# Kernel optimization log

Hardware: AMD Instinct MI355X
Metric: run time of the kernel (lower is better)

## Reference

```python
import jax, jax.numpy as jnp
import numpy as np

N = 50000      # nodes
E = 800000     # edges (avg degree 16)
IN = 128       # input feature dim
HID = 32       # per-head hidden dim
OUT = 64       # per-head output dim
H = 2          # heads per layer
NEG = 0.2      # leaky relu negative slope


def setup_inputs() -> dict:
    key = jax.random.key(0)
    ks = jax.random.split(key, 16)
    x = jax.random.normal(ks[0], (N, IN), dtype=jnp.float32)
    src = jax.random.randint(ks[1], (E,), 0, N)
    dst = jax.random.randint(ks[2], (E,), 0, N)

    def lin(k, fin, fout):
        return jax.random.normal(k, (fin, fout), dtype=jnp.float32) * (1.0 / np.sqrt(fin))

    def attn(k, h, d):
        return jax.random.normal(k, (h, d), dtype=jnp.float32) * 0.1

    # layer 0: IN -> H*HID, layer 1: H*HID -> H*HID, layer 2 (output): H*HID -> H*OUT
    W0, al0, ar0, b0 = lin(ks[3], IN, H * HID), attn(ks[4], H, HID), attn(ks[5], H, HID), jnp.zeros((H * HID,), jnp.float32)
    W1, al1, ar1, b1 = lin(ks[6], H * HID, H * HID), attn(ks[7], H, HID), attn(ks[8], H, HID), jnp.zeros((H * HID,), jnp.float32)
    W2, al2, ar2, b2 = lin(ks[9], H * HID, H * OUT), attn(ks[10], H, OUT), attn(ks[11], H, OUT), jnp.zeros((H * OUT,), jnp.float32)
    return {"x": x, "src": src, "dst": dst,
            "W0": W0, "al0": al0, "ar0": ar0, "b0": b0,
            "W1": W1, "al1": al1, "ar1": ar1, "b1": b1,
            "W2": W2, "al2": al2, "ar2": ar2, "b2": b2}


def gat_conv(x, src, dst, W, al, ar, b, heads, out_dim, apply_relu):
    # feat: [N, H, D]
    feat = (x @ W).reshape(-1, heads, out_dim)
    el = jnp.einsum('nhd,hd->nh', feat, al)   # [N, H]
    er = jnp.einsum('nhd,hd->nh', feat, ar)   # [N, H]
    # per-edge attention logits, leaky-relu
    e = jax.nn.leaky_relu(el[src] + er[dst], NEG)          # [E, H]
    # edge softmax over incoming edges of each dst node (numerically stable)
    m = jax.ops.segment_max(e, dst, num_segments=N)        # [N, H]
    m = jnp.where(jnp.isfinite(m), m, 0.0)                 # nodes w/o in-edges
    ex = jnp.exp(e - m[dst])                               # [E, H]
    s = jax.ops.segment_sum(ex, dst, num_segments=N)       # [N, H]
    alpha = ex / s[dst]                                    # [E, H]
    # weighted aggregate of source features into dst nodes
    rst = jax.ops.segment_sum(feat[src] * alpha[:, :, None], dst, num_segments=N)  # [N, H, D]
    rst = rst + b.reshape(1, heads, out_dim)
    if apply_relu:
        rst = jax.nn.relu(rst)
    return rst


def reference(x, src, dst, W0, al0, ar0, b0, W1, al1, ar1, b1, W2, al2, ar2, b2):
    h = gat_conv(x, src, dst, W0, al0, ar0, b0, H, HID, True).reshape(N, H * HID)   # flatten(1)
    h = gat_conv(h, src, dst, W1, al1, ar1, b1, H, HID, True).reshape(N, H * HID)   # flatten(1)
    logits = gat_conv(h, src, dst, W2, al2, ar2, b2, H, OUT, False).mean(axis=1)    # mean over heads -> [N, OUT]
    return logits
```

## Files before the change

kernel.cpp:

```cpp
#include <hip/hip_runtime.h>
#include <hip/hip_bf16.h>
#include <hip/hip_fp16.h>

#define NNODES 50000
#define NEG_SLOPE 0.2f
#define BKT_SHIFT 8
#define NBKT ((NNODES + 255) >> 8)
#define STRIDE 5120
#define PCHUNK 2048
#define PEPT 8

typedef _Float16 half8 __attribute__((ext_vector_type(8)));
typedef float v4f __attribute__((ext_vector_type(4)));

__device__ __forceinline__ int rfl(int v) { return __builtin_amdgcn_readfirstlane(v); }

__device__ __forceinline__ void pack_one(const float* W, _Float16* Wp, int K, int C, int tid) {
    int KC = K / 32;
    int l = tid & 63;
    int kc = (tid >> 6) % KC;
    int t = tid / (KC * 64);
    int cc = l & 15, q = l >> 4;
    half8 b;
#pragma unroll
    for (int j = 0; j < 8; j++)
        b[j] = (_Float16)W[(size_t)(kc * 32 + q * 8 + j) * C + t * 16 + cc];
    *(half8*)(Wp + (size_t)tid * 8) = b;
}

__global__ __launch_bounds__(256) void kernelAB(
    const float* __restrict__ x, const float* __restrict__ W0,
    const float* __restrict__ AL, const float* __restrict__ AR,
    _Float16* __restrict__ featA, float2* __restrict__ el2A, float2* __restrict__ er2A,
    const float* __restrict__ W2, _Float16* __restrict__ Wp2,
    const int* __restrict__ src, const int* __restrict__ dst,
    int* __restrict__ bcursor, int2* __restrict__ ebuf, int E, int N) {
    int blk = blockIdx.x;
    if (blk >= 786) {
        __shared__ int hist[NBKT];
        __shared__ int gbase[NBKT];
        int t = threadIdx.x;
        for (int i = t; i < NBKT; i += 256) hist[i] = 0;
        __syncthreads();
        int base = (blk - 786) * PCHUNK;
        int sreg[PEPT], dreg[PEPT], rreg[PEPT], breg[PEPT];
#pragma unroll
        for (int k = 0; k < PEPT; k++) {
            int i = base + k * 256 + t;
            if (i < E) {
                sreg[k] = src[i];
                dreg[k] = dst[i];
                breg[k] = dreg[k] >> BKT_SHIFT;
                rreg[k] = atomicAdd(&hist[breg[k]], 1);
            } else {
                breg[k] = -1;
            }
        }
        __syncthreads();
        for (int i = t; i < NBKT; i += 256)
            if (hist[i]) gbase[i] = i * STRIDE + atomicAdd(&bcursor[i * 16], hist[i]);
        __syncthreads();
#pragma unroll
        for (int k = 0; k < PEPT; k++) {
            if (breg[k] >= 0)
                ebuf[(size_t)(gbase[breg[k]] + rreg[k])] = make_int2(sreg[k], dreg[k]);
        }
        return;
    }
    if (blk >= 782) {
        int tid = (blk - 782) * 256 + threadIdx.x;
        if (tid < 8 * 2 * 64) pack_one(W2, Wp2, 64, 128, tid);
        return;
    }
    int wave = threadIdx.x >> 6, lane = threadIdx.x & 63;
    int mtile = blk * 4 + wave;
    if (mtile * 16 >= N) return;
    int m0 = mtile * 16;
    int c = lane & 15, q = lane >> 4;
    v4f acc[4];
#pragma unroll
    for (int t = 0; t < 4; t++) acc[t] = (v4f){0.f, 0.f, 0.f, 0.f};
    const size_t arow = (size_t)(m0 + c) * 128 + q * 8;
#pragma unroll
    for (int kc = 0; kc < 4; kc++) {
        const float* xr = x + arow + kc * 32;
        float4 f0 = *(const float4*)xr;
        float4 f1 = *(const float4*)(xr + 4);
        float fv[8] = {f0.x, f0.y, f0.z, f0.w, f1.x, f1.y, f1.z, f1.w};
        half8 ah, av;
#pragma unroll
        for (int j = 0; j < 8; j++) {
            ah[j] = (_Float16)fv[j];
            av[j] = (_Float16)(fv[j] - (float)ah[j]);
        }
#pragma unroll
        for (int tt = 0; tt < 4; tt++) {
            half8 b;
#pragma unroll
            for (int j = 0; j < 8; j++)
                b[j] = (_Float16)W0[(size_t)(kc * 32 + q * 8 + j) * 64 + tt * 16 + c];
            acc[tt] = __builtin_amdgcn_mfma_f32_16x16x32_f16(ah, b, acc[tt], 0, 0, 0);
            acc[tt] = __builtin_amdgcn_mfma_f32_16x16x32_f16(av, b, acc[tt], 0, 0, 0);
        }
    }
#pragma unroll
    for (int tt = 0; tt < 4; tt++)
#pragma unroll
        for (int r = 0; r < 4; r++) {
            int row = m0 + q * 4 + r;
            featA[(size_t)row * 64 + tt * 16 + c] = (_Float16)acc[tt][r];
        }
    float alv[4], arv[4];
#pragma unroll
    for (int tt = 0; tt < 4; tt++) { alv[tt] = AL[tt * 16 + c]; arv[tt] = AR[tt * 16 + c]; }
#pragma unroll
    for (int r = 0; r < 4; r++) {
        float l0 = 0.f, l1 = 0.f, r0 = 0.f, r1 = 0.f;
#pragma unroll
        for (int tt = 0; tt < 4; tt++) {
            float v = acc[tt][r];
            if (tt < 2) { l0 = fmaf(v, alv[tt], l0); r0 = fmaf(v, arv[tt], r0); }
            else        { l1 = fmaf(v, alv[tt], l1); r1 = fmaf(v, arv[tt], r1); }
        }
#pragma unroll
        for (int m = 1; m < 16; m <<= 1) {
            l0 += __shfl_xor(l0, m, 64);
            l1 += __shfl_xor(l1, m, 64);
            r0 += __shfl_xor(r0, m, 64);
            r1 += __shfl_xor(r1, m, 64);
        }
        if (c == 0) {
            int row = m0 + q * 4 + r;
            el2A[row] = make_float2(l0, l1);
            er2A[row] = make_float2(r0, r1);
        }
    }
}

__global__ __launch_bounds__(256) void local_sort(const int2* __restrict__ ebuf,
                                                  const int* __restrict__ bcursor,
                                                  int2* __restrict__ rowse,
                                                  int* __restrict__ csrc, int N) {
    __shared__ int lcnt[256], lrow[256], ws[4];
    int b = blockIdx.x;
    int d0 = b << BKT_SHIFT;
    int t = threadIdx.x;
    int base = b * STRIDE;
    int endE = base + bcursor[b * 16];
    lcnt[t] = 0;
    __syncthreads();
    for (int i = base + t; i < endE; i += 256)
        atomicAdd(&lcnt[ebuf[i].y - d0], 1);
    __syncthreads();
    int v = lcnt[t];
    int lane = t & 63;
    int x = v;
#pragma unroll
    for (int m = 1; m < 64; m <<= 1) {
        int y = __shfl_up(x, m, 64);
        if (lane >= m) x += y;
    }
    if (lane == 63) ws[t >> 6] = x;
    __syncthreads();
    int w = t >> 6, waveoff = 0;
#pragma unroll
    for (int k = 0; k < 4; k++) if (k < w) waveoff += ws[k];
    int excl = base + waveoff + x - v;
    lrow[t] = excl;
    int d = d0 + t;
    if (d < N) rowse[d] = make_int2(excl, excl + v);
    lcnt[t] = 0;
    __syncthreads();
    for (int i = base + t; i < endE; i += 256) {
        int2 e = ebuf[i];
        int ld = e.y - d0;
        int p = lrow[ld] + atomicAdd(&lcnt[ld], 1);
        csrc[p] = e.x;
    }
}

__global__ __launch_bounds__(256) void agg0_gemm1(
    const int2* __restrict__ rowse, const int* __restrict__ csrc,
    const float2* __restrict__ el2A, const float2* __restrict__ er2A,
    const _Float16* __restrict__ featA, const float* __restrict__ b0,
    const float* __restrict__ W1, const float* __restrict__ al1, const float* __restrict__ ar1,
    _Float16* __restrict__ featB, float2* __restrict__ el2B, float2* __restrict__ er2B,
    int N) {
    __shared__ int2 stA[4][64], stB[4][64];
    __shared__ float vbuf[4][64];
    __shared__ float4 w1v[16 * 64];
    int wave = threadIdx.x >> 6, lane = threadIdx.x & 63, h = lane >> 5;
    for (int i = threadIdx.x; i < 64 * 64; i += 256) {
        int k = i >> 6, cc = i & 63;
        ((float*)w1v)[((((k >> 2) << 6) + cc) << 2) | (k & 3)] = W1[i];
    }
    __syncthreads();
    float bl = b0[lane];
    float al1v = al1[lane], ar1v = ar1[lane];
    const int2* stH = h ? stB[wave] : stA[wave];
    for (int n0 = blockIdx.x * 4 + wave; n0 < N; n0 += gridDim.x * 4) {
        int n = rfl(n0);
        int2 se = rowse[n];
        int beg = rfl(se.x), end = rfl(se.y);
        float2 rr = er2A[n];
        float s = 0.f, acc = 0.f;
        for (int base = beg; base < end; base += 64) {
            int idx = base + lane;
            int sv = 0; float wxv = 0.f, wyv = 0.f;
            if (idx < end) {
                sv = csrc[idx];
                float2 l = el2A[sv];
                float t0 = l.x + rr.x; t0 = t0 > 0.f ? t0 : NEG_SLOPE * t0;
                float t1 = l.y + rr.y; t1 = t1 > 0.f ? t1 : NEG_SLOPE * t1;
                wxv = __expf(t0); wyv = __expf(t1);
            }
            stA[wave][lane] = make_int2(sv, __float_as_int(wxv));
            stB[wave][lane] = make_int2(sv, __float_as_int(wyv));
            int cnt = (min(64, end - base) + 7) & ~7;
            for (int j = 0; j < cnt; j += 8) {
                int4 e01 = *(const int4*)(stH + j);
                int4 e23 = *(const int4*)(stH + j + 2);
                int4 e45 = *(const int4*)(stH + j + 4);
                int4 e67 = *(const int4*)(stH + j + 6);
                float f0 = (float)featA[(size_t)e01.x * 64 + lane];
                float f1 = (float)featA[(size_t)e01.z * 64 + lane];
                float f2 = (float)featA[(size_t)e23.x * 64 + lane];
                float f3 = (float)featA[(size_t)e23.z * 64 + lane];
                float f4 = (float)featA[(size_t)e45.x * 64 + lane];
                float f5 = (float)featA[(size_t)e45.z * 64 + lane];
                float f6 = (float)featA[(size_t)e67.x * 64 + lane];
                float f7 = (float)featA[(size_t)e67.z * 64 + lane];
                float w0 = __int_as_float(e01.y), w1 = __int_as_float(e01.w);
                float w2 = __int_as_float(e23.y), w3 = __int_as_float(e23.w);
                float w4 = __int_as_float(e45.y), w5 = __int_as_float(e45.w);
                float w6 = __int_as_float(e67.y), w7 = __int_as_float(e67.w);
                s += ((w0 + w1) + (w2 + w3)) + ((w4 + w5) + (w6 + w7));
                acc = fmaf(w0, f0, acc);
                acc = fmaf(w1, f1, acc);
                acc = fmaf(w2, f2, acc);
                acc = fmaf(w3, f3, acc);
                acc = fmaf(w4, f4, acc);
                acc = fmaf(w5, f5, acc);
                acc = fmaf(w6, f6, acc);
                acc = fmaf(w7, f7, acc);
            }
        }
        float v = (s > 0.f) ? acc / s : 0.f;
        v = fmaxf(v + bl, 0.f);
        vbuf[wave][lane] = v;
        const float4* vv = (const float4*)vbuf[wave];
        float f = 0.f;
#pragma unroll
        for (int kk = 0; kk < 16; kk++) {
            float4 v4 = vv[kk];
            float4 w4 = w1v[(kk << 6) + lane];
            f = fmaf(v4.x, w4.x, f);
            f = fmaf(v4.y, w4.y, f);
            f = fmaf(v4.z, w4.z, f);
            f = fmaf(v4.w, w4.w, f);
        }
        featB[(size_t)n * 64 + lane] = (_Float16)f;
        float vl = f * al1v, vr = f * ar1v;
#pragma unroll
        for (int m = 1; m < 32; m <<= 1) {
            vl += __shfl_xor(vl, m, 64);
            vr += __shfl_xor(vr, m, 64);
        }
        if ((lane & 31) == 0) {
            ((float*)el2B)[n * 2 + h] = vl;
            ((float*)er2B)[n * 2 + h] = vr;
        }
    }
}

__global__ __launch_bounds__(256) void aggregate32(
    const int2* __restrict__ rowse, const int* __restrict__ csrc,
    const float2* __restrict__ el2, const float2* __restrict__ er2,
    const _Float16* __restrict__ feat16, const float* __restrict__ b,
    _Float16* __restrict__ ahi, _Float16* __restrict__ alo, int N) {
    __shared__ int2 stA[4][64], stB[4][64];
    int wave = threadIdx.x >> 6, lane = threadIdx.x & 63, h = lane >> 5;
    int n = rfl(blockIdx.x * 4 + wave);
    if (n >= N) return;
    float bl = b[lane];
    int2 se = rowse[n];
    int beg = rfl(se.x), end = rfl(se.y);
    float2 rr = er2[n];
    const int2* stH = h ? stB[wave] : stA[wave];
    float s = 0.f, acc = 0.f;
    for (int base = beg; base < end; base += 64) {
        int idx = base + lane;
        int sv = 0; float wxv = 0.f, wyv = 0.f;
        if (idx < end) {
            sv = csrc[idx];
            float2 l = el2[sv];
            float t0 = l.x + rr.x; t0 = t0 > 0.f ? t0 : NEG_SLOPE * t0;
            float t1 = l.y + rr.y; t1 = t1 > 0.f ? t1 : NEG_SLOPE * t1;
            wxv = __expf(t0); wyv = __expf(t1);
        }
        stA[wave][lane] = make_int2(sv, __float_as_int(wxv));
        stB[wave][lane] = make_int2(sv, __float_as_int(wyv));
        int cnt = (min(64, end - base) + 7) & ~7;
        for (int j = 0; j < cnt; j += 8) {
            int4 e01 = *(const int4*)(stH + j);
            int4 e23 = *(const int4*)(stH + j + 2);
            int4 e45 = *(const int4*)(stH + j + 4);
            int4 e67 = *(const int4*)(stH + j + 6);
            float f0 = (float)feat16[(size_t)e01.x * 64 + lane];
            float f1 = (float)feat16[(size_t)e01.z * 64 + lane];
            float f2 = (float)feat16[(size_t)e23.x * 64 + lane];
            float f3 = (float)feat16[(size_t)e23.z * 64 + lane];
            float f4 = (float)feat16[(size_t)e45.x * 64 + lane];
            float f5 = (float)feat16[(size_t)e45.z * 64 + lane];
            float f6 = (float)feat16[(size_t)e67.x * 64 + lane];
            float f7 = (float)feat16[(size_t)e67.z * 64 + lane];
            float w0 = __int_as_float(e01.y), w1 = __int_as_float(e01.w);
            float w2 = __int_as_float(e23.y), w3 = __int_as_float(e23.w);
            float w4 = __int_as_float(e45.y), w5 = __int_as_float(e45.w);
            float w6 = __int_as_float(e67.y), w7 = __int_as_float(e67.w);
            s += ((w0 + w1) + (w2 + w3)) + ((w4 + w5) + (w6 + w7));
            acc = fmaf(w0, f0, acc);
            acc = fmaf(w1, f1, acc);
            acc = fmaf(w2, f2, acc);
            acc = fmaf(w3, f3, acc);
            acc = fmaf(w4, f4, acc);
            acc = fmaf(w5, f5, acc);
            acc = fmaf(w6, f6, acc);
            acc = fmaf(w7, f7, acc);
        }
    }
    float v = (s > 0.f) ? acc / s : 0.f;
    v = fmaxf(v + bl, 0.f);
    _Float16 hv = (_Float16)v;
    ahi[(size_t)n * 64 + lane] = hv;
    alo[(size_t)n * 64 + lane] = (_Float16)(v - (float)hv);
}

__global__ __launch_bounds__(256) void gemm_mfma2(
    const _Float16* __restrict__ Ahi, const _Float16* __restrict__ Alo,
    const _Float16* __restrict__ Wp,
    const float* __restrict__ AL, const float* __restrict__ AR,
    __half2* __restrict__ feat2, float2* __restrict__ el2, float2* __restrict__ er2,
    int N) {
    constexpr int KC = 2, NT = 8;
    int wave = threadIdx.x >> 6, lane = threadIdx.x & 63;
    int mtile = blockIdx.x * 4 + wave;
    if (mtile * 16 >= N) return;
    int m0 = mtile * 16;
    int c = lane & 15, q = lane >> 4;
    v4f acc[NT];
#pragma unroll
    for (int t = 0; t < NT; t++) acc[t] = (v4f){0.f, 0.f, 0.f, 0.f};
    const size_t arow = (size_t)(m0 + c) * 64 + q * 8;
#pragma unroll
    for (int kc = 0; kc < KC; kc++) {
        half8 ah = *(const half8*)(Ahi + arow + kc * 32);
        half8 av = *(const half8*)(Alo + arow + kc * 32);
#pragma unroll
        for (int t = 0; t < NT; t++) {
            half8 b = *(const half8*)(Wp + ((size_t)(t * KC + kc) * 64 + lane) * 8);
            acc[t] = __builtin_amdgcn_mfma_f32_16x16x32_f16(ah, b, acc[t], 0, 0, 0);
            acc[t] = __builtin_amdgcn_mfma_f32_16x16x32_f16(av, b, acc[t], 0, 0, 0);
        }
    }
#pragma unroll
    for (int t = 0; t < NT / 2; t++)
#pragma unroll
        for (int r = 0; r < 4; r++) {
            int row = m0 + q * 4 + r;
            feat2[(size_t)row * 64 + t * 16 + c] =
                __floats2half2_rn(acc[t][r], acc[t + NT / 2][r]);
        }
    float alv[NT], arv[NT];
#pragma unroll
    for (int t = 0; t < NT; t++) { alv[t] = AL[t * 16 + c]; arv[t] = AR[t * 16 + c]; }
#pragma unroll
    for (int r = 0; r < 4; r++) {
        float l0 = 0.f, l1 = 0.f, r0 = 0.f, r1 = 0.f;
#pragma unroll
        for (int t = 0; t < NT; t++) {
            float v = acc[t][r];
            if (t < NT / 2) { l0 = fmaf(v, alv[t], l0); r0 = fmaf(v, arv[t], r0); }
            else            { l1 = fmaf(v, alv[t], l1); r1 = fmaf(v, arv[t], r1); }
        }
#pragma unroll
        for (int m = 1; m < 16; m <<= 1) {
            l0 += __shfl_xor(l0, m, 64);
            l1 += __shfl_xor(l1, m, 64);
            r0 += __shfl_xor(r0, m, 64);
            r1 += __shfl_xor(r1, m, 64);
        }
        if (c == 0) {
            int row = m0 + q * 4 + r;
            el2[row] = make_float2(l0, l1);
            er2[row] = make_float2(r0, r1);
        }
    }
}

__global__ __launch_bounds__(256) void aggregate64_mean(
    const int2* __restrict__ rowse, const int* __restrict__ csrc,
    const float2* __restrict__ el2, const float2* __restrict__ er2,
    const __half2* __restrict__ feat2, const float* __restrict__ b,
    float* __restrict__ out, int N) {
    __shared__ int4 st[4][64];
    int wave = threadIdx.x >> 6, lane = threadIdx.x & 63;
    int n = rfl(blockIdx.x * 4 + wave);
    if (n >= N) return;
    float b0 = b[lane], b1 = b[64 + lane];
    int2 se = rowse[n];
    int beg = rfl(se.x), end = rfl(se.y);
    float2 rr = er2[n];
    float s0 = 0.f, s1 = 0.f, a0 = 0.f, a1 = 0.f;
    for (int base = beg; base < end; base += 64) {
        int idx = base + lane;
        int sv = 0; float wxv = 0.f, wyv = 0.f;
        if (idx < end) {
            sv = csrc[idx];
            float2 l = el2[sv];
            float t0 = l.x + rr.x; t0 = t0 > 0.f ? t0 : NEG_SLOPE * t0;
            float t1 = l.y + rr.y; t1 = t1 > 0.f ? t1 : NEG_SLOPE * t1;
            wxv = __expf(t0); wyv = __expf(t1);
        }
        st[wave][lane] = make_int4(sv, __float_as_int(wxv), __float_as_int(wyv), 0);
        int cnt = (min(64, end - base) + 7) & ~7;
        for (int j = 0; j < cnt; j += 8) {
            float2 fv[8]; float wxs[8], wys[8];
#pragma unroll
            for (int u = 0; u < 8; u++) {
                int4 e = st[wave][j + u];
                wxs[u] = __int_as_float(e.y);
                wys[u] = __int_as_float(e.z);
                fv[u] = __half22float2(feat2[(size_t)e.x * 64 + lane]);
            }
#pragma unroll
            for (int u = 0; u < 8; u++) {
                s0 += wxs[u]; s1 += wys[u];
                a0 = fmaf(wxs[u], fv[u].x, a0);
                a1 = fmaf(wys[u], fv[u].y, a1);
            }
        }
    }
    float v0 = (s0 > 0.f) ? a0 / s0 : 0.f;
    float v1 = (s1 > 0.f) ? a1 / s1 : 0.f;
    out[(size_t)n * 64 + lane] = 0.5f * ((v0 + b0) + (v1 + b1));
}


extern "C" void kernel_launch(void* const* d_in, const int* in_sizes, int n_in,
                              void* d_out, int out_size, void* d_ws, size_t ws_size,
                              hipStream_t stream) {
    const float* x   = (const float*)d_in[0];
    const int*   src = (const int*)d_in[1];
    const int*   dst = (const int*)d_in[2];
    const float* W0  = (const float*)d_in[3];
    const float* al0 = (const float*)d_in[4];
    const float* ar0 = (const float*)d_in[5];
    const float* b0  = (const float*)d_in[6];
    const float* W1  = (const float*)d_in[7];
    const float* al1 = (const float*)d_in[8];
    const float* ar1 = (const float*)d_in[9];
    const float* b1  = (const float*)d_in[10];
    const float* W2  = (const float*)d_in[11];
    const float* al2 = (const float*)d_in[12];
    const float* ar2 = (const float*)d_in[13];
    const float* b2  = (const float*)d_in[14];
    float* out = (float*)d_out;

    const int N = NNODES;
    const int E = in_sizes[1];

    char* p = (char*)d_ws;
    auto alloc = [&](size_t bytes) {
        void* r = (void*)p;
        p += (bytes + 255) & ~(size_t)255;
        return r;
    };
    int*    bcursor = (int*)alloc((size_t)NBKT * 16 * 4);
    int2*   rowse   = (int2*)alloc((size_t)N * 8);
    int2*   ebuf    = (int2*)alloc(((size_t)NBKT * STRIDE + 4096) * 8);
    int*    csrc    = (int*)alloc(((size_t)NBKT * STRIDE + 4096) * 4);
    float2* el2A    = (float2*)alloc((size_t)N * 8);
    float2* er2A    = (float2*)alloc((size_t)N * 8);
    float2* el2B    = (float2*)alloc((size_t)N * 8);
    float2* er2B    = (float2*)alloc((size_t)N * 8);
    _Float16* ahi   = (_Float16*)alloc((size_t)N * 64 * 2);
    _Float16* alo   = (_Float16*)alloc((size_t)N * 64 * 2);
    void*   featA   = alloc((size_t)N * 64 * 4);
    _Float16* featB = (_Float16*)alloc((size_t)N * 64 * 2);
    _Float16* Wp2   = (_Float16*)alloc(8 * 2 * 64 * 8 * 2);

    hipMemsetAsync(bcursor, 0, (size_t)NBKT * 16 * 4, stream);
    int nch = (E + PCHUNK - 1) / PCHUNK;
    kernelAB<<<786 + nch, 256, 0, stream>>>(x, W0, al0, ar0, (_Float16*)featA, el2A, er2A,
                                            W2, Wp2, src, dst, bcursor, ebuf, E, N);
    local_sort<<<NBKT, 256, 0, stream>>>(ebuf, bcursor, rowse, csrc, N);

    int nb4 = (N + 3) / 4;
    agg0_gemm1<<<2048, 256, 0, stream>>>(rowse, csrc, el2A, er2A, (const _Float16*)featA,
                                         b0, W1, al1, ar1, featB, el2B, er2B, N);
    aggregate32<<<nb4, 256, 0, stream>>>(rowse, csrc, el2B, er2B, featB, b1, ahi, alo, N);
    int gb = (N / 16 + 3) / 4;
    gemm_mfma2<<<gb, 256, 0, stream>>>(ahi, alo, Wp2, al2, ar2, (__half2*)featA, el2A, er2A, N);
    aggregate64_mean<<<nb4, 256, 0, stream>>>(rowse, csrc, el2A, er2A, (const __half2*)featA,
                                              b2, out, N);
}
```

Before: 226.9 us.

## Process two destination nodes per wave in aggregation kernels, widen local sort

```diff
diff --git a/kernel.cpp b/kernel.cpp
--- a/kernel.cpp
+++ b/kernel.cpp
@@ -137,22 +137,22 @@
     }
 }
 
-__global__ __launch_bounds__(256) void local_sort(const int2* __restrict__ ebuf,
-                                                  const int* __restrict__ bcursor,
-                                                  int2* __restrict__ rowse,
-                                                  int* __restrict__ csrc, int N) {
+__global__ __launch_bounds__(1024) void local_sort(const int2* __restrict__ ebuf,
+                                                   const int* __restrict__ bcursor,
+                                                   int2* __restrict__ rowse,
+                                                   int* __restrict__ csrc, int N) {
     __shared__ int lcnt[256], lrow[256], ws[4];
     int b = blockIdx.x;
     int d0 = b << BKT_SHIFT;
     int t = threadIdx.x;
     int base = b * STRIDE;
     int endE = base + bcursor[b * 16];
-    lcnt[t] = 0;
+    if (t < 256) lcnt[t] = 0;
     __syncthreads();
-    for (int i = base + t; i < endE; i += 256)
+    for (int i = base + t; i < endE; i += 1024)
         atomicAdd(&lcnt[ebuf[i].y - d0], 1);
     __syncthreads();
-    int v = lcnt[t];
+    int v = (t < 256) ? lcnt[t] : 0;
     int lane = t & 63;
     int x = v;
 #pragma unroll
@@ -160,18 +160,20 @@
         int y = __shfl_up(x, m, 64);
         if (lane >= m) x += y;
     }
-    if (lane == 63) ws[t >> 6] = x;
+    if (t < 256 && lane == 63) ws[t >> 6] = x;
     __syncthreads();
-    int w = t >> 6, waveoff = 0;
-#pragma unroll
-    for (int k = 0; k < 4; k++) if (k < w) waveoff += ws[k];
-    int excl = base + waveoff + x - v;
-    lrow[t] = excl;
-    int d = d0 + t;
-    if (d < N) rowse[d] = make_int2(excl, excl + v);
-    lcnt[t] = 0;
+    if (t < 256) {
+        int w = t >> 6, waveoff = 0;
+#pragma unroll
+        for (int k = 0; k < 4; k++) if (k < w) waveoff += ws[k];
+        int excl = base + waveoff + x - v;
+        lrow[t] = excl;
+        int d = d0 + t;
+        if (d < N) rowse[d] = make_int2(excl, excl + v);
+        lcnt[t] = 0;
+    }
     __syncthreads();
-    for (int i = base + t; i < endE; i += 256) {
+    for (int i = base + t; i < endE; i += 1024) {
         int2 e = ebuf[i];
         int ld = e.y - d0;
         int p = lrow[ld] + atomicAdd(&lcnt[ld], 1);
@@ -278,34 +280,58 @@
     const float2* __restrict__ el2, const float2* __restrict__ er2,
     const _Float16* __restrict__ feat16, const float* __restrict__ b,
     _Float16* __restrict__ ahi, _Float16* __restrict__ alo, int N) {
-    __shared__ int2 stA[4][64], stB[4][64];
+    __shared__ int2 stA0[4][64], stB0[4][64], stA1[4][64], stB1[4][64];
     int wave = threadIdx.x >> 6, lane = threadIdx.x & 63, h = lane >> 5;
-    int n = rfl(blockIdx.x * 4 + wave);
-    if (n >= N) return;
+    int g = rfl(blockIdx.x * 4 + wave);
+    int n0 = 2 * g, n1 = n0 + 1;
+    if (n0 >= N) return;
+    bool has1 = (n1 < N);
     float bl = b[lane];
-    int2 se = rowse[n];
-    int beg = rfl(se.x), end = rfl(se.y);
-    float2 rr = er2[n];
-    const int2* stH = h ? stB[wave] : stA[wave];
-    float s = 0.f, acc = 0.f;
-    for (int base = beg; base < end; base += 64) {
-        int idx = base + lane;
-        int sv = 0; float wxv = 0.f, wyv = 0.f;
-        if (idx < end) {
-            sv = csrc[idx];
-            float2 l = el2[sv];
-            float t0 = l.x + rr.x; t0 = t0 > 0.f ? t0 : NEG_SLOPE * t0;
-            float t1 = l.y + rr.y; t1 = t1 > 0.f ? t1 : NEG_SLOPE * t1;
-            wxv = __expf(t0); wyv = __expf(t1);
-        }
-        stA[wave][lane] = make_int2(sv, __float_as_int(wxv));
-        stB[wave][lane] = make_int2(sv, __float_as_int(wyv));
-        int cnt = (min(64, end - base) + 7) & ~7;
+    int2 se0 = rowse[n0];
+    int2 se1 = has1 ? rowse[n1] : make_int2(0, 0);
+    int beg0 = rfl(se0.x), len0 = rfl(se0.y) - beg0;
+    int beg1 = rfl(se1.x), len1 = rfl(se1.y) - beg1;
+    float2 rr0 = er2[n0];
+    float2 rr1 = has1 ? er2[n1] : make_float2(0.f, 0.f);
+    const int2* stH0 = h ? stB0[wave] : stA0[wave];
+    const int2* stH1 = h ? stB1[wave] : stA1[wave];
+    float s0 = 0.f, acc0 = 0.f, s1 = 0.f, acc1 = 0.f;
+    int chunks = max(len0, len1);
+    for (int off = 0; off < chunks; off += 64) {
+        {
+            int sv = 0; float wxv = 0.f, wyv = 0.f;
+            if (off + lane < len0) {
+                sv = csrc[beg0 + off + lane];
+                float2 l = el2[sv];
+                float t0 = l.x + rr0.x; t0 = t0 > 0.f ? t0 : NEG_SLOPE * t0;
+                float t1 = l.y + rr0.y; t1 = t1 > 0.f ? t1 : NEG_SLOPE * t1;
+                wxv = __expf(t0); wyv = __expf(t1);
+            }
+            stA0[wave][lane] = make_int2(sv, __float_as_int(wxv));
+            stB0[wave][lane] = make_int2(sv, __float_as_int(wyv));
+        }
+        {
+            int sv = 0; float wxv = 0.f, wyv = 0.f;
+            if (off + lane < len1) {
+                sv = csrc[beg1 + off + lane];
+                float2 l = el2[sv];
+                float t0 = l.x + rr1.x; t0 = t0 > 0.f ? t0 : NEG_SLOPE * t0;
+                float t1 = l.y + rr1.y; t1 = t1 > 0.f ? t1 : NEG_SLOPE * t1;
+                wxv = __expf(t0); wyv = __expf(t1);
+            }
+            stA1[wave][lane] = make_int2(sv, __float_as_int(wxv));
+            stB1[wave][lane] = make_int2(sv, __float_as_int(wyv));
+        }
+        int cnt = (min(64, chunks - off) + 7) & ~7;
         for (int j = 0; j < cnt; j += 8) {
-            int4 e01 = *(const int4*)(stH + j);
-            int4 e23 = *(const int4*)(stH + j + 2);
-            int4 e45 = *(const int4*)(stH + j + 4);
-            int4 e67 = *(const int4*)(stH + j + 6);
+            int4 e01 = *(const int4*)(stH0 + j);
+            int4 e23 = *(const int4*)(stH0 + j + 2);
+            int4 e45 = *(const int4*)(stH0 + j + 4);
+            int4 e67 = *(const int4*)(stH0 + j + 6);
+            int4 g01 = *(const int4*)(stH1 + j);
+            int4 g23 = *(const int4*)(stH1 + j + 2);
+            int4 g45 = *(const int4*)(stH1 + j + 4);
+            int4 g67 = *(const int4*)(stH1 + j + 6);
             float f0 = (float)feat16[(size_t)e01.x * 64 + lane];
             float f1 = (float)feat16[(size_t)e01.z * 64 + lane];
             float f2 = (float)feat16[(size_t)e23.x * 64 + lane];
@@ -314,26 +340,54 @@
             float f5 = (float)feat16[(size_t)e45.z * 64 + lane];
             float f6 = (float)feat16[(size_t)e67.x * 64 + lane];
             float f7 = (float)feat16[(size_t)e67.z * 64 + lane];
+            float p0 = (float)feat16[(size_t)g01.x * 64 + lane];
+            float p1 = (float)feat16[(size_t)g01.z * 64 + lane];
+            float p2 = (float)feat16[(size_t)g23.x * 64 + lane];
+            float p3 = (float)feat16[(size_t)g23.z * 64 + lane];
+            float p4 = (float)feat16[(size_t)g45.x * 64 + lane];
+            float p5 = (float)feat16[(size_t)g45.z * 64 + lane];
+            float p6 = (float)feat16[(size_t)g67.x * 64 + lane];
+            float p7 = (float)feat16[(size_t)g67.z * 64 + lane];
             float w0 = __int_as_float(e01.y), w1 = __int_as_float(e01.w);
             float w2 = __int_as_float(e23.y), w3 = __int_as_float(e23.w);
             float w4 = __int_as_float(e45.y), w5 = __int_as_float(e45.w);
             float w6 = __int_as_float(e67.y), w7 = __int_as_float(e67.w);
-            s += ((w0 + w1) + (w2 + w3)) + ((w4 + w5) + (w6 + w7));
-            acc = fmaf(w0, f0, acc);
-            acc = fmaf(w1, f1, acc);
-            acc = fmaf(w2, f2, acc);
-            acc = fmaf(w3, f3, acc);
-            acc = fmaf(w4, f4, acc);
-            acc = fmaf(w5, f5, acc);
-            acc = fmaf(w6, f6, acc);
-            acc = fmaf(w7, f7, acc);
-        }
-    }
-    float v = (s > 0.f) ? acc / s : 0.f;
+            float x0 = __int_as_float(g01.y), x1 = __int_as_float(g01.w);
+            float x2 = __int_as_float(g23.y), x3 = __int_as_float(g23.w);
+            float x4 = __int_as_float(g45.y), x5 = __int_as_float(g45.w);
+            float x6 = __int_as_float(g67.y), x7 = __int_as_float(g67.w);
+            s0 += ((w0 + w1) + (w2 + w3)) + ((w4 + w5) + (w6 + w7));
+            acc0 = fmaf(w0, f0, acc0);
+            acc0 = fmaf(w1, f1, acc0);
+            acc0 = fmaf(w2, f2, acc0);
+            acc0 = fmaf(w3, f3, acc0);
+            acc0 = fmaf(w4, f4, acc0);
+            acc0 = fmaf(w5, f5, acc0);
+            acc0 = fmaf(w6, f6, acc0);
+            acc0 = fmaf(w7, f7, acc0);
+            s1 += ((x0 + x1) + (x2 + x3)) + ((x4 + x5) + (x6 + x7));
+            acc1 = fmaf(x0, p0, acc1);
+            acc1 = fmaf(x1, p1, acc1);
+            acc1 = fmaf(x2, p2, acc1);
+            acc1 = fmaf(x3, p3, acc1);
+            acc1 = fmaf(x4, p4, acc1);
+            acc1 = fmaf(x5, p5, acc1);
+            acc1 = fmaf(x6, p6, acc1);
+            acc1 = fmaf(x7, p7, acc1);
+        }
+    }
+    float v = (s0 > 0.f) ? acc0 / s0 : 0.f;
     v = fmaxf(v + bl, 0.f);
     _Float16 hv = (_Float16)v;
-    ahi[(size_t)n * 64 + lane] = hv;
-    alo[(size_t)n * 64 + lane] = (_Float16)(v - (float)hv);
+    ahi[(size_t)n0 * 64 + lane] = hv;
+    alo[(size_t)n0 * 64 + lane] = (_Float16)(v - (float)hv);
+    if (has1) {
+        float u = (s1 > 0.f) ? acc1 / s1 : 0.f;
+        u = fmaxf(u + bl, 0.f);
+        _Float16 hu = (_Float16)u;
+        ahi[(size_t)n1 * 64 + lane] = hu;
+        alo[(size_t)n1 * 64 + lane] = (_Float16)(u - (float)hu);
+    }
 }
 
 __global__ __launch_bounds__(256) void gemm_mfma2(
@@ -403,47 +457,85 @@
     const float2* __restrict__ el2, const float2* __restrict__ er2,
     const __half2* __restrict__ feat2, const float* __restrict__ b,
     float* __restrict__ out, int N) {
-    __shared__ int4 st[4][64];
+    __shared__ int4 st0[4][64], st1[4][64];
     int wave = threadIdx.x >> 6, lane = threadIdx.x & 63;
-    int n = rfl(blockIdx.x * 4 + wave);
-    if (n >= N) return;
-    float b0 = b[lane], b1 = b[64 + lane];
-    int2 se = rowse[n];
-    int beg = rfl(se.x), end = rfl(se.y);
-    float2 rr = er2[n];
-    float s0 = 0.f, s1 = 0.f, a0 = 0.f, a1 = 0.f;
-    for (int base = beg; base < end; base += 64) {
-        int idx = base + lane;
-        int sv = 0; float wxv = 0.f, wyv = 0.f;
-        if (idx < end) {
-            sv = csrc[idx];
-            float2 l = el2[sv];
-            float t0 = l.x + rr.x; t0 = t0 > 0.f ? t0 : NEG_SLOPE * t0;
-            float t1 = l.y + rr.y; t1 = t1 > 0.f ? t1 : NEG_SLOPE * t1;
-            wxv = __expf(t0); wyv = __expf(t1);
-        }
-        st[wave][lane] = make_int4(sv, __float_as_int(wxv), __float_as_int(wyv), 0);
-        int cnt = (min(64, end - base) + 7) & ~7;
+    int g = rfl(blockIdx.x * 4 + wave);
+    int n0 = 2 * g, n1 = n0 + 1;
+    if (n0 >= N) return;
+    bool has1 = (n1 < N);
+    float b0v = b[lane], b1v = b[64 + lane];
+    int2 se0 = rowse[n0];
+    int2 se1 = has1 ? rowse[n1] : make_int2(0, 0);
+    int beg0 = rfl(se0.x), len0 = rfl(se0.y) - beg0;
+    int beg1 = rfl(se1.x), len1 = rfl(se1.y) - beg1;
+    float2 rr0 = er2[n0];
+    float2 rr1 = has1 ? er2[n1] : make_float2(0.f, 0.f);
+    float s00 = 0.f, s01 = 0.f, a00 = 0.f, a01 = 0.f;
+    float s10 = 0.f, s11 = 0.f, a10 = 0.f, a11 = 0.f;
+    int chunks = max(len0, len1);
+    for (int off = 0; off < chunks; off += 64) {
+        {
+            int sv = 0; float wxv = 0.f, wyv = 0.f;
+            if (off + lane < len0) {
+                sv = csrc[beg0 + off + lane];
+                float2 l = el2[sv];
+                float t0 = l.x + rr0.x; t0 = t0 > 0.f ? t0 : NEG_SLOPE * t0;
+                float t1 = l.y + rr0.y; t1 = t1 > 0.f ? t1 : NEG_SLOPE * t1;
+                wxv = __expf(t0); wyv = __expf(t1);
+            }
+            st0[wave][lane] = make_int4(sv, __float_as_int(wxv), __float_as_int(wyv), 0);
+        }
+        {
+            int sv = 0; float wxv = 0.f, wyv = 0.f;
+            if (off + lane < len1) {
+                sv = csrc[beg1 + off + lane];
+                float2 l = el2[sv];
+                float t0 = l.x + rr1.x; t0 = t0 > 0.f ? t0 : NEG_SLOPE * t0;
+                float t1 = l.y + rr1.y; t1 = t1 > 0.f ? t1 : NEG_SLOPE * t1;
+                wxv = __expf(t0); wyv = __expf(t1);
+            }
+            st1[wave][lane] = make_int4(sv, __float_as_int(wxv), __float_as_int(wyv), 0);
+        }
+        int cnt = (min(64, chunks - off) + 7) & ~7;
         for (int j = 0; j < cnt; j += 8) {
-            float2 fv[8]; float wxs[8], wys[8];
+            float2 fv0[8], fv1[8];
+            float wx0[8], wy0[8], wx1[8], wy1[8];
 #pragma unroll
             for (int u = 0; u < 8; u++) {
-                int4 e = st[wave][j + u];
-                wxs[u] = __int_as_float(e.y);
-                wys[u] = __int_as_float(e.z);
-                fv[u] = __half22float2(feat2[(size_t)e.x * 64 + lane]);
+                int4 e = st0[wave][j + u];
+                wx0[u] = __int_as_float(e.y);
+                wy0[u] = __int_as_float(e.z);
+                fv0[u] = __half22float2(feat2[(size_t)e.x * 64 + lane]);
             }
 #pragma unroll
             for (int u = 0; u < 8; u++) {
-                s0 += wxs[u]; s1 += wys[u];
-                a0 = fmaf(wxs[u], fv[u].x, a0);
-                a1 = fmaf(wys[u], fv[u].y, a1);
-            }
-        }
-    }
-    float v0 = (s0 > 0.f) ? a0 / s0 : 0.f;
-    float v1 = (s1 > 0.f) ? a1 / s1 : 0.f;
-    out[(size_t)n * 64 + lane] = 0.5f * ((v0 + b0) + (v1 + b1));
+                int4 e = st1[wave][j + u];
+                wx1[u] = __int_as_float(e.y);
+                wy1[u] = __int_as_float(e.z);
+                fv1[u] = __half22float2(feat2[(size_t)e.x * 64 + lane]);
+            }
+#pragma unroll
+            for (int u = 0; u < 8; u++) {
+                s00 += wx0[u]; s01 += wy0[u];
+                a00 = fmaf(wx0[u], fv0[u].x, a00);
+                a01 = fmaf(wy0[u], fv0[u].y, a01);
+            }
+#pragma unroll
+            for (int u = 0; u < 8; u++) {
+                s10 += wx1[u]; s11 += wy1[u];
+                a10 = fmaf(wx1[u], fv1[u].x, a10);
+                a11 = fmaf(wy1[u], fv1[u].y, a11);
+            }
+        }
+    }
+    float v0 = (s00 > 0.f) ? a00 / s00 : 0.f;
+    float v1 = (s01 > 0.f) ? a01 / s01 : 0.f;
+    out[(size_t)n0 * 64 + lane] = 0.5f * ((v0 + b0v) + (v1 + b1v));
+    if (has1) {
+        float u0 = (s10 > 0.f) ? a10 / s10 : 0.f;
+        float u1 = (s11 > 0.f) ? a11 / s11 : 0.f;
+        out[(size_t)n1 * 64 + lane] = 0.5f * ((u0 + b0v) + (u1 + b1v));
+    }
 }
 
 
@@ -494,14 +586,15 @@
     int nch = (E + PCHUNK - 1) / PCHUNK;
     kernelAB<<<786 + nch, 256, 0, stream>>>(x, W0, al0, ar0, (_Float16*)featA, el2A, er2A,
                                             W2, Wp2, src, dst, bcursor, ebuf, E, N);
-    local_sort<<<NBKT, 256, 0, stream>>>(ebuf, bcursor, rowse, csrc, N);
-
-    int nb4 = (N + 3) / 4;
-    agg0_gemm1<<<2048, 256, 0, stream>>>(rowse, csrc, el2A, er2A, (const _Float16*)featA,
+    local_sort<<<NBKT, 1024, 0, stream>>>(ebuf, bcursor, rowse, csrc, N);
+
+    agg0_gemm1<<<4096, 256, 0, stream>>>(rowse, csrc, el2A, er2A, (const _Float16*)featA,
                                          b0, W1, al1, ar1, featB, el2B, er2B, N);
-    aggregate32<<<nb4, 256, 0, stream>>>(rowse, csrc, el2B, er2B, featB, b1, ahi, alo, N);
+    int npair = (N + 1) / 2;
+    int nbp = (npair + 3) / 4;
+    aggregate32<<<nbp, 256, 0, stream>>>(rowse, csrc, el2B, er2B, featB, b1, ahi, alo, N);
     int gb = (N / 16 + 3) / 4;
     gemm_mfma2<<<gb, 256, 0, stream>>>(ahi, alo, Wp2, al2, ar2, (__half2*)featA, el2A, er2A, N);
-    aggregate64_mean<<<nb4, 256, 0, stream>>>(rowse, csrc, el2A, er2A, (const __half2*)featA,
+    aggregate64_mean<<<nbp, 256, 0, stream>>>(rowse, csrc, el2A, er2A, (const __half2*)featA,
                                               b2, out, N);
 }
```

Result: no change. 226.1 us (-0.4%).
